# Kernel tuning notes

Hardware: AMD Instinct MI355X
Metric: run time of the kernel (lower is better)

## Reference

```python
import jax, jax.numpy as jnp
import numpy as np

VTH = 1.0  # config['v_threshold']
DT = 1.0


def spike_fn(x):
    # forward of ActFun_adp: heaviside(mem - vth)
    return (x > 0).astype(x.dtype)


def setup_inputs() -> dict:
    key = jax.random.key(0)
    k0, k1, k2, k3, k4 = jax.random.split(key, 5)
    B, T, D, H, O = 256, 250, 700, 1024, 20
    input_data = jax.random.normal(k0, (B, T, D), dtype=jnp.float32)
    # dense_1: nn.Linear(700, hidden) default init ~ U(-1/sqrt(D), 1/sqrt(D)); normal/sqrt(D) is an equivalent-scale stand-in
    W1 = jax.random.normal(k1, (H, D), dtype=jnp.float32) / np.sqrt(D).astype(np.float32)
    b1 = jnp.zeros((H,), dtype=jnp.float32)
    tau_m1 = jax.random.uniform(k2, (H,), dtype=jnp.float32, minval=0.0, maxval=4.0)
    # dense_2: xavier_normal_ weight, zero bias
    W2 = jax.random.normal(k3, (O, H), dtype=jnp.float32) * np.sqrt(2.0 / (H + O)).astype(np.float32)
    b2 = jnp.zeros((O,), dtype=jnp.float32)
    tau_m2 = jax.random.uniform(k4, (O,), dtype=jnp.float32, minval=0.0, maxval=4.0)
    return {"input_data": input_data, "W1": W1, "b1": b1, "tau_m1": tau_m1,
            "W2": W2, "b2": b2, "tau_m2": tau_m2}


def reference(input_data, W1, b1, tau_m1, W2, b2, tau_m2):
    B, T, D = input_data.shape
    H = W1.shape[0]
    O = W2.shape[0]
    alpha1 = jax.nn.sigmoid(tau_m1)  # [H]
    alpha2 = jax.nn.sigmoid(tau_m2)  # [O]
    # dense_1 is time-invariant: precompute projections for all timesteps [T,B,H]
    d1_all = (jnp.einsum('btd,hd->bth', input_data, W1) + b1).transpose(1, 0, 2)

    def step(carry, xs):
        mem1, spk1, mem2, acc = carry
        d1_t, i = xs
        # LIF layer 1: soft reset via -vth*spike (mem_update_pra, R_m=1, dt=1)
        mem1 = mem1 * alpha1 + (1.0 - alpha1) * d1_t - VTH * spk1 * DT
        spk1 = spike_fn(mem1 - VTH)
        # readout integrator
        d2 = spk1 @ W2.T + b2
        mem2 = mem2 * alpha2 + (1.0 - alpha2) * d2
        # accumulate softmax for i > 10
        gate = jnp.where(i > 10, jnp.float32(1.0), jnp.float32(0.0))
        acc = acc + gate * jax.nn.softmax(mem2, axis=1)
        return (mem1, spk1, mem2, acc), None

    init = (jnp.zeros((B, H), jnp.float32), jnp.zeros((B, H), jnp.float32),
            jnp.zeros((B, O), jnp.float32), jnp.zeros((B, O), jnp.float32))
    (_, _, _, acc), _ = jax.lax.scan(step, init, (d1_all, jnp.arange(T)))
    return acc
```

## Files before the change

### kernel.cpp

```cpp
#include <hip/hip_runtime.h>
#include <hip/hip_bf16.h>

#define B_  256
#define T_  250
#define D_  700
#define H_  1024
#define O_  20
#define KP  704
#define M_  64000
#define NT  22

typedef __attribute__((ext_vector_type(8))) short bf16x8;
typedef __attribute__((ext_vector_type(4))) float f32x4;

__device__ __forceinline__ void gl_lds16(const void* g, void* l) {
    __builtin_amdgcn_global_load_lds(
        (const __attribute__((address_space(1))) unsigned int*)g,
        (__attribute__((address_space(3))) unsigned int*)l, 16, 0, 0);
}

__global__ void split_convert(const float* __restrict__ src,
                              unsigned short* __restrict__ hi,
                              unsigned short* __restrict__ lo,
                              int M, int Kin, int Kout)
{
    int idx = blockIdx.x * blockDim.x + threadIdx.x;
    int chunks = Kout >> 3;
    int total = M * chunks;
    if (idx >= total) return;
    int m  = idx / chunks;
    int c  = idx - m * chunks;
    int d0 = c << 3;
    float x[8];
    if (d0 + 8 <= Kin) {
        const float4* p = (const float4*)(src + (long)m * Kin + d0);
        float4 v0 = p[0], v1 = p[1];
        x[0] = v0.x; x[1] = v0.y; x[2] = v0.z; x[3] = v0.w;
        x[4] = v1.x; x[5] = v1.y; x[6] = v1.z; x[7] = v1.w;
    } else {
#pragma unroll
        for (int e = 0; e < 8; ++e) {
            int d = d0 + e;
            x[e] = (d < Kin) ? src[(long)m * Kin + d] : 0.0f;
        }
    }
    unsigned short h8[8], l8[8];
#pragma unroll
    for (int e = 0; e < 8; ++e) {
        __hip_bfloat16 h = __float2bfloat16(x[e]);
        float hf = __bfloat162float(h);
        __hip_bfloat16 lv = __float2bfloat16(x[e] - hf);
        h8[e] = *(unsigned short*)&h;
        l8[e] = *(unsigned short*)&lv;
    }
    long ob = (long)m * Kout + d0;
    *(uint4*)(hi + ob) = *(uint4*)h8;
    *(uint4*)(lo + ob) = *(uint4*)l8;
}

#define MF(a,b,c) (c) = __builtin_amdgcn_mfma_f32_16x16x32_bf16((a),(b),(c),0,0,0)
#define MF4(a, bb, accp) do { \
    MF(a, bb[0], accp[0]); MF(a, bb[1], accp[1]); \
    MF(a, bb[2], accp[2]); MF(a, bb[3], accp[3]); } while (0)
#define PIN() __builtin_amdgcn_sched_barrier(0)
#define LGKM(n) do { \
    asm volatile("s_waitcnt lgkmcnt(" #n ")" ::: "memory"); PIN(); } while (0)

__global__ __launch_bounds__(512, 2) void gemm256(
    const unsigned short* __restrict__ Ahi, const unsigned short* __restrict__ Alo,
    const unsigned short* __restrict__ Bhi, const unsigned short* __restrict__ Blo,
    const float* __restrict__ bias, float* __restrict__ C)
{
    __shared__ __align__(16) unsigned short sAh[2 * 8192];
    __shared__ __align__(16) unsigned short sAl[2 * 8192];
    __shared__ __align__(16) unsigned short sBh[2 * 8192];
    __shared__ __align__(16) unsigned short sBl[2 * 8192];

    const int bid = blockIdx.x;
    const int wg  = (bid & 7) * 125 + (bid >> 3);
    const int mblk = wg >> 2;
    const int nblk = wg & 3;

    const int t    = threadIdx.x;
    const int wave = t >> 6, lane = t & 63;
    const int wr = wave >> 2, wc = wave & 3;

    const int  rowoff = lane >> 2;
    const int  slotl  = (lane & 3) ^ ((lane >> 3) & 3);
    const long GCH    = 16L * KP;
    const long gA     = (long)(mblk * 256 + rowoff) * KP + slotl * 8;
    const long gB     = (long)(nblk * 256 + rowoff) * KP + slotl * 8;
    const int  ldsO   = lane * 8;
    const int  cB0 = 2 * wave, cB1 = 2 * wave + 1;
    const int  cA0 = (wave < 4) ? wave : wave + 4;
    const int  cA1 = cA0 + 4;

    const unsigned short* gBh = Bhi + gB;
    const unsigned short* gBl = Blo + gB;
    const unsigned short* gAh = Ahi + gA;
    const unsigned short* gAl = Alo + gA;

    auto issueB = [&](long ko, int bufo) {
        gl_lds16(gBh + (long)cB0 * GCH + ko, &sBh[bufo + cB0 * 512 + ldsO]);
        gl_lds16(gBh + (long)cB1 * GCH + ko, &sBh[bufo + cB1 * 512 + ldsO]);
        gl_lds16(gBl + (long)cB0 * GCH + ko, &sBl[bufo + cB0 * 512 + ldsO]);
        gl_lds16(gBl + (long)cB1 * GCH + ko, &sBl[bufo + cB1 * 512 + ldsO]);
    };
    auto issueA0 = [&](long ko, int bufo) {
        gl_lds16(gAh + (long)cA0 * GCH + ko, &sAh[bufo + cA0 * 512 + ldsO]);
        gl_lds16(gAl + (long)cA0 * GCH + ko, &sAl[bufo + cA0 * 512 + ldsO]);
    };
    auto issueA1 = [&](long ko, int bufo) {
        gl_lds16(gAh + (long)cA1 * GCH + ko, &sAh[bufo + cA1 * 512 + ldsO]);
        gl_lds16(gAl + (long)cA1 * GCH + ko, &sAl[bufo + cA1 * 512 + ldsO]);
    };

    const int fr   = lane & 15, fq = lane >> 4;
    const int fxor = ((fq ^ ((fr >> 1) & 3)) << 3);
    const int abase = (wr * 128 + fr) * 32 + fxor;
    const int bbase = (wc * 64 + fr) * 32 + fxor;

    f32x4 acc[8][4];
#pragma unroll
    for (int i = 0; i < 8; ++i)
#pragma unroll
        for (int j = 0; j < 4; ++j) acc[i][j] = (f32x4){0.f, 0.f, 0.f, 0.f};

    issueB(0, 0); issueA0(0, 0); issueA1(0, 0);

    for (int tt = 0; tt < NT; ++tt) {
        const int  cur = (tt & 1) ? 8192 : 0;
        const int  nxt = 8192 - cur;
        const long ksn = (long)(tt + 1) * 32;
        const bool pf  = (tt + 1 < NT);

        asm volatile("s_waitcnt vmcnt(2)" ::: "memory");
        __builtin_amdgcn_s_barrier();
        bf16x8 bh[4], bl[4];
        bh[0] = *(const bf16x8*)&sBh[cur + bbase + 0 * 512];
        bh[1] = *(const bf16x8*)&sBh[cur + bbase + 1 * 512];
        bh[2] = *(const bf16x8*)&sBh[cur + bbase + 2 * 512];
        bh[3] = *(const bf16x8*)&sBh[cur + bbase + 3 * 512];
        bf16x8 a0h = *(const bf16x8*)&sAh[cur + abase + 0 * 512];
        PIN();
        bf16x8 a1h = *(const bf16x8*)&sAh[cur + abase + 1 * 512];
        PIN();
        bf16x8 a0l = *(const bf16x8*)&sAl[cur + abase + 0 * 512];
        PIN();
        bf16x8 a1l = *(const bf16x8*)&sAl[cur + abase + 1 * 512];
        PIN();
        bl[0] = *(const bf16x8*)&sBl[cur + bbase + 0 * 512];
        bl[1] = *(const bf16x8*)&sBl[cur + bbase + 1 * 512];
        bl[2] = *(const bf16x8*)&sBl[cur + bbase + 2 * 512];
        bl[3] = *(const bf16x8*)&sBl[cur + bbase + 3 * 512];
        PIN();
        bf16x8 a2h = *(const bf16x8*)&sAh[cur + abase + 2 * 512];
        PIN();
        bf16x8 a3h = *(const bf16x8*)&sAh[cur + abase + 3 * 512];
        PIN();
        bf16x8 a2l = *(const bf16x8*)&sAl[cur + abase + 2 * 512];
        PIN();
        bf16x8 a3l = *(const bf16x8*)&sAl[cur + abase + 3 * 512];
        PIN();
        if (pf) issueB(ksn, nxt);
        __builtin_amdgcn_s_setprio(1);
        LGKM(11); MF4(a0h, bh, acc[0]); PIN();
        LGKM(10); MF4(a1h, bh, acc[1]); PIN();
        LGKM(9);  MF4(a0l, bh, acc[0]); PIN();
        LGKM(8);  MF4(a1l, bh, acc[1]); PIN();
        LGKM(4);  MF4(a0h, bl, acc[0]); MF4(a1h, bl, acc[1]); PIN();
        __builtin_amdgcn_s_setprio(0);
        if (pf) issueA0(ksn, nxt);
        __builtin_amdgcn_s_setprio(1);
        LGKM(3);  MF4(a2h, bh, acc[2]); PIN();
        LGKM(2);  MF4(a3h, bh, acc[3]); PIN();
        LGKM(1);  MF4(a2l, bh, acc[2]); PIN();
        LGKM(0);  MF4(a3l, bh, acc[3]);
                  MF4(a2h, bl, acc[2]); MF4(a3h, bl, acc[3]); PIN();
        __builtin_amdgcn_s_setprio(0);

        if (pf) { asm volatile("s_waitcnt vmcnt(6)" ::: "memory"); }
        else    { asm volatile("s_waitcnt vmcnt(0)" ::: "memory"); }
        __builtin_amdgcn_s_barrier();
        bf16x8 a4h = *(const bf16x8*)&sAh[cur + abase + 4 * 512];
        PIN();
        bf16x8 a5h = *(const bf16x8*)&sAh[cur + abase + 5 * 512];
        PIN();
        bf16x8 a4l = *(const bf16x8*)&sAl[cur + abase + 4 * 512];
        PIN();
        bf16x8 a5l = *(const bf16x8*)&sAl[cur + abase + 5 * 512];
        PIN();
        bf16x8 a6h = *(const bf16x8*)&sAh[cur + abase + 6 * 512];
        PIN();
        bf16x8 a7h = *(const bf16x8*)&sAh[cur + abase + 7 * 512];
        PIN();
        bf16x8 a6l = *(const bf16x8*)&sAl[cur + abase + 6 * 512];
        PIN();
        bf16x8 a7l = *(const bf16x8*)&sAl[cur + abase + 7 * 512];
        PIN();
        if (pf) issueA1(ksn, nxt);
        __builtin_amdgcn_s_setprio(1);
        LGKM(7); MF4(a4h, bh, acc[4]); PIN();
        LGKM(6); MF4(a5h, bh, acc[5]); PIN();
        LGKM(5); MF4(a4l, bh, acc[4]); PIN();
        LGKM(4); MF4(a5l, bh, acc[5]);
                 MF4(a4h, bl, acc[4]); MF4(a5h, bl, acc[5]); PIN();
        LGKM(3); MF4(a6h, bh, acc[6]); PIN();
        LGKM(2); MF4(a7h, bh, acc[7]); PIN();
        LGKM(1); MF4(a6l, bh, acc[6]); PIN();
        LGKM(0); MF4(a7l, bh, acc[7]);
                 MF4(a6h, bl, acc[6]); MF4(a7h, bl, acc[7]); PIN();
        __builtin_amdgcn_s_setprio(0);
    }

    const int r0 = mblk * 256 + wr * 128 + fq * 4;
    const int cc = nblk * 256 + wc * 64 + fr;
#pragma unroll
    for (int j = 0; j < 4; ++j) {
        int col = cc + j * 16;
        float bv = bias[col];
#pragma unroll
        for (int i = 0; i < 8; ++i) {
            int row = r0 + i * 16;
#pragma unroll
            for (int r = 0; r < 4; ++r)
                C[(long)(row + r) * H_ + col] = acc[i][j][r] + bv;
        }
    }
}

__global__ __launch_bounds__(256) void lif_spikes(
    const float* __restrict__ d1,
    const float* __restrict__ tau1,
    unsigned long long* __restrict__ spk)
{
    const int b    = blockIdx.y;
    const int h    = blockIdx.x * 256 + threadIdx.x;
    const int lane = threadIdx.x & 63;
    const int widx = blockIdx.x * 4 + (threadIdx.x >> 6);

    float tv  = tau1[h];
    float a1  = 1.0f / (1.0f + __expf(-tv));
    float om1 = 1.0f - a1;
    float mem = 0.f, sp = 0.f;

    const float* dp = d1 + (long)b * T_ * H_ + h;
    unsigned long long* op = spk + (long)b * T_ * 16 + widx;

    float p0 = dp[0],        p1 = dp[1L * H_], p2 = dp[2L * H_];
    float p3 = dp[3L * H_],  p4 = dp[4L * H_], p5 = dp[5L * H_];

    for (int ts = 0; ts < T_; ++ts) {
        float cur = p0;
        p0 = p1; p1 = p2; p2 = p3; p3 = p4; p4 = p5;
        int nts = ts + 6; nts = (nts < T_) ? nts : (T_ - 1);
        p5 = dp[(long)nts * H_];

        mem = mem * a1 + om1 * cur - sp;
        sp  = (mem > 1.0f) ? 1.0f : 0.0f;
        unsigned long long msk = __ballot(mem > 1.0f);
        if (lane == 0) op[(long)ts * 16] = msk;
    }
}

__global__ __launch_bounds__(256) void readout_dots(
    const unsigned long long* __restrict__ spk,
    const float* __restrict__ W2,
    float* __restrict__ d2t)
{
    const int t = threadIdx.x, wave = t >> 6, lane = t & 63;

    float w2r[5][16];
#pragma unroll
    for (int oo = 0; oo < 5; ++oo)
#pragma unroll
        for (int q = 0; q < 4; ++q)
            *(float4*)&w2r[oo][4 * q] =
                *(const float4*)&W2[(wave * 5 + oo) * H_ + lane * 16 + 4 * q];

    const int rbase = blockIdx.x * 32;
    int b0 = rbase / T_;
    int ts0 = rbase - b0 * T_;

    for (int i = 0; i < 32; i += 2) {
        int r0 = rbase + i, r1 = r0 + 1;
        unsigned long long bw0 = spk[(long)r0 * 16 + (lane >> 2)];
        unsigned long long bw1 = spk[(long)r1 * 16 + (lane >> 2)];
        unsigned int bits0 = (unsigned int)(bw0 >> ((lane & 3) * 16)) & 0xFFFFu;
        unsigned int bits1 = (unsigned int)(bw1 >> ((lane & 3) * 16)) & 0xFFFFu;
        float pa0[5] = {0, 0, 0, 0, 0}, pa1[5] = {0, 0, 0, 0, 0};
#pragma unroll
        for (int j = 0; j < 16; ++j) {
            float f0 = (bits0 >> j) & 1u ? 1.0f : 0.0f;
            float f1 = (bits1 >> j) & 1u ? 1.0f : 0.0f;
#pragma unroll
            for (int oo = 0; oo < 5; ++oo) {
                pa0[oo] = fmaf(f0, w2r[oo][j], pa0[oo]);
                pa1[oo] = fmaf(f1, w2r[oo][j], pa1[oo]);
            }
        }
#pragma unroll
        for (int m = 1; m < 64; m <<= 1)
#pragma unroll
            for (int oo = 0; oo < 5; ++oo) {
                pa0[oo] += __shfl_xor(pa0[oo], m, 64);
                pa1[oo] += __shfl_xor(pa1[oo], m, 64);
            }
        if (lane == 0) {
            int bA = b0, tsA = ts0 + i;
            if (tsA >= T_) { tsA -= T_; bA += 1; }
            int bB = bA, tsB = tsA + 1;
            if (tsB >= T_) { tsB = 0; bB += 1; }
#pragma unroll
            for (int oo = 0; oo < 5; ++oo) {
                d2t[(long)(wave * 5 + oo) * M_ + tsA * 256 + bA] = pa0[oo];
                d2t[(long)(wave * 5 + oo) * M_ + tsB * 256 + bB] = pa1[oo];
            }
        }
    }
}

__global__ __launch_bounds__(64) void mem2_scan(
    const float* __restrict__ d2t,
    const float* __restrict__ tau2, const float* __restrict__ b2,
    float* __restrict__ m2t)
{
    const int o = blockIdx.x;
    const int b = blockIdx.y * 64 + threadIdx.x;
    float tv  = tau2[o];
    float a2  = 1.0f / (1.0f + __expf(-tv));
    float om2 = 1.0f - a2;
    float bv  = b2[o];

    const float* dp = d2t + (long)o * M_ + b;
    float*       mp = m2t + (long)o * M_ + b;
    float mem = 0.f;

    float p0 = dp[0], p1 = dp[256], p2 = dp[512], p3 = dp[768];
    for (int ts = 0; ts < T_; ++ts) {
        float cur = p0; p0 = p1; p1 = p2; p2 = p3;
        int nts = ts + 4; nts = (nts < T_) ? nts : (T_ - 1);
        p3 = dp[(long)nts * 256];
        mem = mem * a2 + om2 * (cur + bv);
        mp[(long)ts * 256] = mem;
    }
}

__global__ __launch_bounds__(256) void softmax_acc(
    const float* __restrict__ m2t,
    float* __restrict__ out)
{
    __shared__ float sp[T_][O_];
    const int b  = blockIdx.x;
    const int ts = threadIdx.x;

    if (ts < T_) {
        if (ts > 10) {
            float m[O_];
#pragma unroll
            for (int o = 0; o < O_; ++o)
                m[o] = m2t[(long)o * M_ + ts * 256 + b];
            float mx = m[0];
#pragma unroll
            for (int o = 1; o < O_; ++o) mx = fmaxf(mx, m[o]);
            float s = 0.f;
#pragma unroll
            for (int o = 0; o < O_; ++o) { m[o] = __expf(m[o] - mx); s += m[o]; }
            float inv = 1.0f / s;
#pragma unroll
            for (int o = 0; o < O_; ++o) sp[ts][o] = m[o] * inv;
        } else {
#pragma unroll
            for (int o = 0; o < O_; ++o) sp[ts][o] = 0.f;
        }
    }
    __syncthreads();
    if (ts < O_) {
        float s = 0.f;
        for (int k = 11; k < T_; ++k) s += sp[k][ts];
        out[b * O_ + ts] = s;
    }
}

extern "C" void kernel_launch(void* const* d_in, const int* in_sizes, int n_in,
                              void* d_out, int out_size, void* d_ws, size_t ws_size,
                              hipStream_t stream)
{
    const float* X    = (const float*)d_in[0];
    const float* W1   = (const float*)d_in[1];
    const float* b1   = (const float*)d_in[2];
    const float* tau1 = (const float*)d_in[3];
    const float* W2   = (const float*)d_in[4];
    const float* b2   = (const float*)d_in[5];
    const float* tau2 = (const float*)d_in[6];
    float* out = (float*)d_out;

    unsigned short* Xhi  = (unsigned short*)d_ws;
    unsigned short* Xlo  = Xhi + (long)M_ * KP;
    unsigned short* W1hi = Xlo + (long)M_ * KP;
    unsigned short* W1lo = W1hi + (long)H_ * KP;
    float* d1 = (float*)(W1lo + (long)H_ * KP);

    unsigned long long* spk = (unsigned long long*)Xhi;
    float* d2t = (float*)Xlo;
    float* m2t = d2t + (long)O_ * M_;

    {
        int chunks = M_ * (KP / 8);
        split_convert<<<(chunks + 255) / 256, 256, 0, stream>>>(X, Xhi, Xlo, M_, D_, KP);
    }
    {
        int chunks = H_ * (KP / 8);
        split_convert<<<(chunks + 255) / 256, 256, 0, stream>>>(W1, W1hi, W1lo, H_, D_, KP);
    }

    gemm256<<<dim3(1000), dim3(512), 0, stream>>>(Xhi, Xlo, W1hi, W1lo, b1, d1);

    {
        dim3 grid(H_ / 256, B_);
        lif_spikes<<<grid, 256, 0, stream>>>(d1, tau1, spk);
    }

    readout_dots<<<M_ / 32, 256, 0, stream>>>(spk, W2, d2t);

    {
        dim3 grid(O_, 4);
        mem2_scan<<<grid, 64, 0, stream>>>(d2t, tau2, b2, m2t);
    }

    softmax_acc<<<B_, 256, 0, stream>>>(m2t, out);
}
```

Baseline: 702.5 us.

## Fuse X bf16 hi/lo split conversion into GEMM A-tile loading

Removes the separate split_convert pass over the large input X. The GEMM now loads fp32 X directly into registers, splits each value into bf16 hi and lo parts, and writes both to LDS inside the pipelined main loop, zero-filling the padded K tail. This saves a full read and write round trip of the bf16 copies of X. In exchange, the A tile no longer uses direct global-to-LDS loads, the GEMM does extra VALU conversion work, and an extra barrier is added per iteration.

```diff
diff --git a/kernel.cpp b/kernel.cpp
--- a/kernel.cpp
+++ b/kernel.cpp
@@ -67,7 +67,7 @@
     asm volatile("s_waitcnt lgkmcnt(" #n ")" ::: "memory"); PIN(); } while (0)
 
 __global__ __launch_bounds__(512, 2) void gemm256(
-    const unsigned short* __restrict__ Ahi, const unsigned short* __restrict__ Alo,
+    const float* __restrict__ X,
     const unsigned short* __restrict__ Bhi, const unsigned short* __restrict__ Blo,
     const float* __restrict__ bias, float* __restrict__ C)
 {
@@ -87,9 +87,10 @@
 
     const int  rowoff = lane >> 2;
     const int  slotl  = (lane & 3) ^ ((lane >> 3) & 3);
+    const int  slotk  = slotl * 8;
     const long GCH    = 16L * KP;
-    const long gA     = (long)(mblk * 256 + rowoff) * KP + slotl * 8;
-    const long gB     = (long)(nblk * 256 + rowoff) * KP + slotl * 8;
+    const long gB     = (long)(nblk * 256 + rowoff) * KP + slotk;
+    const long gX     = (long)(mblk * 256 + rowoff) * D_ + slotk;
     const int  ldsO   = lane * 8;
     const int  cB0 = 2 * wave, cB1 = 2 * wave + 1;
     const int  cA0 = (wave < 4) ? wave : wave + 4;
@@ -97,8 +98,6 @@
 
     const unsigned short* gBh = Bhi + gB;
     const unsigned short* gBl = Blo + gB;
-    const unsigned short* gAh = Ahi + gA;
-    const unsigned short* gAl = Alo + gA;
 
     auto issueB = [&](long ko, int bufo) {
         gl_lds16(gBh + (long)cB0 * GCH + ko, &sBh[bufo + cB0 * 512 + ldsO]);
@@ -106,13 +105,26 @@
         gl_lds16(gBl + (long)cB0 * GCH + ko, &sBl[bufo + cB0 * 512 + ldsO]);
         gl_lds16(gBl + (long)cB1 * GCH + ko, &sBl[bufo + cB1 * 512 + ldsO]);
     };
-    auto issueA0 = [&](long ko, int bufo) {
-        gl_lds16(gAh + (long)cA0 * GCH + ko, &sAh[bufo + cA0 * 512 + ldsO]);
-        gl_lds16(gAl + (long)cA0 * GCH + ko, &sAl[bufo + cA0 * 512 + ldsO]);
+    auto loadA = [&](long koE, int c, float4& r0, float4& r1) {
+        const float* p = X + gX + (long)c * (16L * D_) + koE;
+        r0 = *(const float4*)p;
+        int k1 = (int)koE + slotk + 4;
+        r1 = (float4){0.f, 0.f, 0.f, 0.f};
+        if (k1 + 4 <= D_) r1 = *(const float4*)(p + 4);
     };
-    auto issueA1 = [&](long ko, int bufo) {
-        gl_lds16(gAh + (long)cA1 * GCH + ko, &sAh[bufo + cA1 * 512 + ldsO]);
-        gl_lds16(gAl + (long)cA1 * GCH + ko, &sAl[bufo + cA1 * 512 + ldsO]);
+    auto splitWrite = [&](float4 r0, float4 r1, int bufo, int c) {
+        float xs[8] = {r0.x, r0.y, r0.z, r0.w, r1.x, r1.y, r1.z, r1.w};
+        unsigned short h8[8], l8[8];
+#pragma unroll
+        for (int e = 0; e < 8; ++e) {
+            __hip_bfloat16 h = __float2bfloat16(xs[e]);
+            float hf = __bfloat162float(h);
+            __hip_bfloat16 lv = __float2bfloat16(xs[e] - hf);
+            h8[e] = *(unsigned short*)&h;
+            l8[e] = *(unsigned short*)&lv;
+        }
+        *(uint4*)&sAh[bufo + c * 512 + ldsO] = *(uint4*)h8;
+        *(uint4*)&sAl[bufo + c * 512 + ldsO] = *(uint4*)l8;
     };
 
     const int fr   = lane & 15, fq = lane >> 4;
@@ -126,7 +138,18 @@
 #pragma unroll
         for (int j = 0; j < 4; ++j) acc[i][j] = (f32x4){0.f, 0.f, 0.f, 0.f};
 
-    issueB(0, 0); issueA0(0, 0); issueA1(0, 0);
+    float4 a0r0, a0r1, a1r0, a1r1;
+
+    issueB(0, 0);
+    loadA(0, cA0, a0r0, a0r1);
+    loadA(0, cA1, a1r0, a1r1);
+    PIN();
+    asm volatile("s_waitcnt vmcnt(2)" ::: "memory");
+    PIN();
+    splitWrite(a0r0, a0r1, 0, cA0);
+    asm volatile("s_waitcnt lgkmcnt(0)" ::: "memory");
+    PIN();
+    __builtin_amdgcn_s_barrier();
 
     for (int tt = 0; tt < NT; ++tt) {
         const int  cur = (tt & 1) ? 8192 : 0;
@@ -134,8 +157,6 @@
         const long ksn = (long)(tt + 1) * 32;
         const bool pf  = (tt + 1 < NT);
 
-        asm volatile("s_waitcnt vmcnt(2)" ::: "memory");
-        __builtin_amdgcn_s_barrier();
         bf16x8 bh[4], bl[4];
         bh[0] = *(const bf16x8*)&sBh[cur + bbase + 0 * 512];
         bh[1] = *(const bf16x8*)&sBh[cur + bbase + 1 * 512];
@@ -170,7 +191,8 @@
         LGKM(8);  MF4(a1l, bh, acc[1]); PIN();
         LGKM(4);  MF4(a0h, bl, acc[0]); MF4(a1h, bl, acc[1]); PIN();
         __builtin_amdgcn_s_setprio(0);
-        if (pf) issueA0(ksn, nxt);
+        if (pf) loadA(ksn, cA0, a0r0, a0r1);
+        PIN();
         __builtin_amdgcn_s_setprio(1);
         LGKM(3);  MF4(a2h, bh, acc[2]); PIN();
         LGKM(2);  MF4(a3h, bh, acc[3]); PIN();
@@ -181,7 +203,12 @@
 
         if (pf) { asm volatile("s_waitcnt vmcnt(6)" ::: "memory"); }
         else    { asm volatile("s_waitcnt vmcnt(0)" ::: "memory"); }
+        PIN();
+        splitWrite(a1r0, a1r1, cur, cA1);
+        asm volatile("s_waitcnt lgkmcnt(0)" ::: "memory");
+        PIN();
         __builtin_amdgcn_s_barrier();
+
         bf16x8 a4h = *(const bf16x8*)&sAh[cur + abase + 4 * 512];
         PIN();
         bf16x8 a5h = *(const bf16x8*)&sAh[cur + abase + 5 * 512];
@@ -198,7 +225,8 @@
         PIN();
         bf16x8 a7l = *(const bf16x8*)&sAl[cur + abase + 7 * 512];
         PIN();
-        if (pf) issueA1(ksn, nxt);
+        if (pf) loadA(ksn, cA1, a1r0, a1r1);
+        PIN();
         __builtin_amdgcn_s_setprio(1);
         LGKM(7); MF4(a4h, bh, acc[4]); PIN();
         LGKM(6); MF4(a5h, bh, acc[5]); PIN();
@@ -211,6 +239,15 @@
         LGKM(0); MF4(a7l, bh, acc[7]);
                  MF4(a6h, bl, acc[6]); MF4(a7h, bl, acc[7]); PIN();
         __builtin_amdgcn_s_setprio(0);
+
+        if (pf) {
+            asm volatile("s_waitcnt vmcnt(2)" ::: "memory");
+            PIN();
+            splitWrite(a0r0, a0r1, nxt, cA0);
+            asm volatile("s_waitcnt lgkmcnt(0)" ::: "memory");
+            PIN();
+            __builtin_amdgcn_s_barrier();
+        }
     }
 
     const int r0 = mblk * 256 + wr * 128 + fq * 4;
@@ -406,15 +443,11 @@
     float* m2t = d2t + (long)O_ * M_;
 
     {
-        int chunks = M_ * (KP / 8);
-        split_convert<<<(chunks + 255) / 256, 256, 0, stream>>>(X, Xhi, Xlo, M_, D_, KP);
-    }
-    {
         int chunks = H_ * (KP / 8);
         split_convert<<<(chunks + 255) / 256, 256, 0, stream>>>(W1, W1hi, W1lo, H_, D_, KP);
     }
 
-    gemm256<<<dim3(1000), dim3(512), 0, stream>>>(Xhi, Xlo, W1hi, W1lo, b1, d1);
+    gemm256<<<dim3(1000), dim3(512), 0, stream>>>(X, W1hi, W1lo, b1, d1);
 
     {
         dim3 grid(H_ / 256, B_);
```

Measured after the change: 670.5 us. -4.5%, faster.
